# Kernel optimization log

Measured on AMD Instinct MI355X. Metric: run time of the kernel, lower is better.

## Reference

```python
import jax, jax.numpy as jnp
import numpy as np

D, K, STRIDE, PADDING = 5, 3, 1, 2
B, CIN, COUT, H, W = 32, 128, 256, 56, 56


def _conv(x, w, stride, padding):
    return jax.lax.conv_general_dilated(
        x, w, window_strides=(stride, stride),
        padding=[(padding, padding), (padding, padding)],
        dimension_numbers=("NCHW", "OIHW", "NCHW"))


def setup_inputs() -> dict:
    key = jax.random.key(0)
    k1, k2, k3 = jax.random.split(key, 3)
    x = jax.random.normal(k1, (B, CIN, H, W), dtype=jnp.float32)
    # kaiming-uniform-ish core init
    fan_in = CIN * K * K
    bound = float(np.sqrt(6.0 / fan_in))
    core = jax.random.uniform(k2, (COUT, CIN, K, K), dtype=jnp.float32,
                              minval=-bound, maxval=bound)
    periphery = jax.random.uniform(k3, (D * D - K * K,), dtype=jnp.float32,
                                   minval=-0.1, maxval=0.1)
    thresh = jnp.ones((COUT,), jnp.float32) * 0.1
    scale = jnp.array([10.0], jnp.float32)
    return {"x": x, "core": core, "periphery": periphery,
            "thresh": thresh, "scale": scale}


def reference(x, core, periphery, thresh, scale):
    pad = (D - K) // 2  # offset of the KxK core inside the DxD window
    # Dense core conv: embed KxK core at the center of a DxD kernel so core
    # and periphery share the same output grid (padding=PADDING for DxD).
    core_full = jnp.pad(core, ((0, 0), (0, 0), (pad, pad), (pad, pad)))
    core_out = _conv(x, core_full, STRIDE, PADDING)  # [B, COUT, Ho, Wo]

    # Periphery: one shared scalar per off-core offset, shared across all
    # in/out channels -> sum input over channels, conv with a 1x1-channel
    # DxD stencil whose core region is zero.
    periph_mask = np.ones((D, D), dtype=bool)
    periph_mask[pad:pad + K, pad:pad + K] = False
    periph_idx = np.flatnonzero(periph_mask)  # row-major off-core offsets
    pk = jnp.zeros((D * D,), x.dtype).at[periph_idx].set(periphery)
    pk = pk.reshape(1, 1, D, D)
    xs = jnp.sum(x, axis=1, keepdims=True)  # [B,1,H,W]
    periph_out = _conv(xs, pk, STRIDE, PADDING)  # [B,1,Ho,Wo]

    # Per-out-channel threshold/scale gating: periphery term is switched on
    # where the core response exceeds the channel threshold (soft gate).
    gate = jax.nn.sigmoid(scale[0] * (core_out - thresh[None, :, None, None]))
    return core_out + gate * periph_out
```

## Files before the change

kernel.cpp:

```cpp
#include <hip/hip_runtime.h>

typedef __attribute__((__ext_vector_type__(8))) _Float16 f16x8;
typedef __attribute__((__ext_vector_type__(4))) float f32x4;
typedef __attribute__((__ext_vector_type__(4))) int i32x4;

#define HW 56
#define HW2 3136
#define CIN 128
#define COUT 256
#define NB 32
#define NPIX 100352
#define PH 58

static __device__ __forceinline__ unsigned short f2h(float f) {
  _Float16 h = (_Float16)f;
  return __builtin_bit_cast(unsigned short, h);
}

#define GLD_LDS16(g, l)                                          \
  __builtin_amdgcn_global_load_lds(                              \
      (const __attribute__((address_space(1))) void*)(g),        \
      (__attribute__((address_space(3))) void*)(l), 16, 0, 0)

__global__ __launch_bounds__(256) void zero_halo(unsigned short* __restrict__ xp) {
  int t = blockIdx.x * 256 + threadIdx.x;
  int ck = t & 15;
  int pi = t >> 4;
  int b = pi / 228, r = pi - b * 228;
  int h, w;
  if (r < 58) { h = 0; w = r; }
  else if (r < 116) { h = 57; w = r - 58; }
  else { int q = r - 116; h = 1 + (q >> 1); w = (q & 1) * 57; }
  size_t off = (((size_t)(b * PH + h) * PH + w) << 8) + (ck << 4);
  *reinterpret_cast<i32x4*>((char*)xp + off) = (i32x4){0, 0, 0, 0};
}

__global__ __launch_bounds__(256) void prep_x(const float* __restrict__ x,
                                              unsigned short* __restrict__ xp,
                                              float* __restrict__ xs) {
  __shared__ float tile[CIN * 57];
  const int bh = blockIdx.x;
  const float* src = x + (size_t)(bh / HW) * CIN * HW2 + (size_t)(bh % HW) * HW;
  for (int idx = threadIdx.x; idx < CIN * HW; idx += 256) {
    int c = idx / HW, w = idx - c * HW;
    tile[c * 57 + w] = src[(size_t)c * HW2 + w];
  }
  __syncthreads();
  unsigned short* dst =
      xp + (((size_t)(bh / HW) * PH + (bh % HW) + 1) * PH + 1) * CIN;
  for (int idx = threadIdx.x; idx < HW * (CIN / 2); idx += 256) {
    int w = idx >> 6;
    int c = (idx & 63) << 1;
    unsigned lo = f2h(tile[c * 57 + w]);
    unsigned hi = f2h(tile[(c + 1) * 57 + w]);
    *reinterpret_cast<unsigned*>(&dst[w * CIN + c]) = lo | (hi << 16);
  }
  if (threadIdx.x < HW) {
    float s = 0.f;
    for (int c = 0; c < CIN; ++c) s += tile[c * 57 + threadIdx.x];
    xs[(size_t)bh * HW + threadIdx.x] = s;
  }
}

__global__ __launch_bounds__(256) void prep_w(const float* __restrict__ core,
                                              unsigned short* __restrict__ w_t) {
  int i = blockIdx.x * 256 + threadIdx.x;
  int c = i & 127;
  int p = (i >> 7) % 9;
  int m = i / (9 * 128);
  w_t[i] = f2h(core[(size_t)(m * CIN + c) * 9 + p]);
}

__global__ __launch_bounds__(256) void periph_k(const float* __restrict__ xs,
                                                const float* __restrict__ per,
                                                float* __restrict__ po) {
  int n = blockIdx.x * 256 + threadIdx.x;
  int b = n / HW2, r = n - b * HW2;
  int ho = r / HW, wo = r - ho * HW;
  const float* xb = xs + (size_t)b * HW2;
  const int pdy[16] = {0,0,0,0,0,1,1,2,2,3,3,4,4,4,4,4};
  const int pdx[16] = {0,1,2,3,4,0,4,0,4,0,4,0,1,2,3,4};
  float acc = 0.f;
#pragma unroll
  for (int t = 0; t < 16; ++t) {
    int h = ho + pdy[t] - 2, w = wo + pdx[t] - 2;
    if ((unsigned)h < HW && (unsigned)w < HW) acc += per[t] * xb[h * HW + w];
  }
  po[n] = acc;
}

__global__ __launch_bounds__(512, 2) void gemm_k(const unsigned short* __restrict__ xp,
                                                 const unsigned short* __restrict__ w_t,
                                                 const float* __restrict__ po,
                                                 const float* __restrict__ thresh,
                                                 const float* __restrict__ scale,
                                                 float* __restrict__ out) {
  __shared__ __align__(16) char sMem[2 * 65536 + 1024];

  const int tid = threadIdx.x;
  const int lane = tid & 63;
  const int wid = tid >> 6;
  const int wm = wid >> 2;
  const int wn = wid & 3;

  const int bid = blockIdx.x;
  const int n0 = ((bid & 7) * 49 + (bid >> 3)) << 8;

  float* sTh = (float*)(sMem + 131072);
  if (tid < 256) sTh[tid] = thresh[tid];

  const int slot = tid & 7;
  const int trow = tid >> 3;
  const int sw = (slot ^ (trow & 7)) << 4;
  const char* xpc = (const char*)xp;
  const char* wtc = (const char*)w_t;
  int aOff[4], bOff[4];
#pragma unroll
  for (int q = 0; q < 4; ++q) {
    int row = q * 64 + trow;
    aOff[q] = row * (9 * 256) + sw;
    int n = n0 + row;
    int b = n / HW2, rr = n - b * HW2;
    int h = rr / HW, w = rr - h * HW;
    bOff[q] = ((b * PH + h + 1) * PH + (w + 1)) * 256 + sw;
  }
  const int ldsw = wid * 1024;

  int aro[8][2], bro[4][2];
#pragma unroll
  for (int i = 0; i < 8; ++i)
#pragma unroll
    for (int ko = 0; ko < 2; ++ko) {
      int rowA = wm * 128 + i * 16 + (lane & 15);
      int boc = ko * 64 + ((lane >> 4) << 4);
      aro[i][ko] = rowA * 128 + (boc ^ ((rowA & 7) << 4));
    }
#pragma unroll
  for (int j = 0; j < 4; ++j)
#pragma unroll
    for (int ko = 0; ko < 2; ++ko) {
      int rowB = wn * 64 + j * 16 + (lane & 15);
      int boc = ko * 64 + ((lane >> 4) << 4);
      bro[j][ko] = 32768 + rowB * 128 + (boc ^ ((rowB & 7) << 4));
    }

  auto STAGE = [&](int buf, int step) {
    const int p = step >> 1;
    const int c0b = (step & 1) << 7;
    const int dy = p / 3 - 1, dx = p - (p / 3) * 3 - 1;
    const int offA = (p << 8) + c0b;
    const int offB = ((dy * PH + dx) << 8) + c0b;
    char* base = sMem + buf * 65536;
#pragma unroll
    for (int q = 0; q < 4; ++q)
      GLD_LDS16(wtc + aOff[q] + offA, base + ldsw + q * 8192);
#pragma unroll
    for (int q = 0; q < 4; ++q)
      GLD_LDS16(xpc + bOff[q] + offB, base + 32768 + ldsw + q * 8192);
  };

  f32x4 acc[8][4] = {};

  STAGE(0, 0);
  __syncthreads();

#pragma unroll
  for (int s = 0; s < 18; ++s) {
    const char* base = sMem + (s & 1) * 65536;
    __builtin_amdgcn_s_barrier();
    if (s < 17) {
      STAGE((s + 1) & 1, s + 1);
      asm volatile("s_waitcnt vmcnt(8)" ::: "memory");
    } else {
      asm volatile("s_waitcnt vmcnt(0)" ::: "memory");
    }
    __builtin_amdgcn_s_barrier();
    f16x8 bfr[4][2];
#pragma unroll
    for (int j = 0; j < 4; ++j)
#pragma unroll
      for (int ko = 0; ko < 2; ++ko)
        bfr[j][ko] = *reinterpret_cast<const f16x8*>(base + bro[j][ko]);
#pragma unroll
    for (int i = 0; i < 8; ++i) {
      f16x8 a0 = *reinterpret_cast<const f16x8*>(base + aro[i][0]);
      f16x8 a1 = *reinterpret_cast<const f16x8*>(base + aro[i][1]);
      __builtin_amdgcn_s_setprio(1);
#pragma unroll
      for (int j = 0; j < 4; ++j) {
        acc[i][j] = __builtin_amdgcn_mfma_f32_16x16x32_f16(a0, bfr[j][0], acc[i][j], 0, 0, 0);
        acc[i][j] = __builtin_amdgcn_mfma_f32_16x16x32_f16(a1, bfr[j][1], acc[i][j], 0, 0, 0);
      }
      __builtin_amdgcn_s_setprio(0);
    }
  }

  const float sc = scale[0];
#pragma unroll
  for (int j = 0; j < 4; ++j) {
    int n = n0 + wn * 64 + j * 16 + (lane & 15);
    int b = n / HW2;
    int r = n - b * HW2;
    float pv = po[n];
    float* op = out + (size_t)b * (COUT * HW2) + r;
#pragma unroll
    for (int i = 0; i < 8; ++i) {
      int cl = wm * 128 + i * 16 + ((lane >> 4) << 2);
#pragma unroll
      for (int q = 0; q < 4; ++q) {
        float cv = acc[i][j][q];
        float g = 1.f / (1.f + __expf(-sc * (cv - sTh[cl + q])));
        op[(size_t)(cl + q) * HW2] = cv + g * pv;
      }
    }
  }
}

extern "C" void kernel_launch(void* const* d_in, const int* in_sizes, int n_in,
                              void* d_out, int out_size, void* d_ws, size_t ws_size,
                              hipStream_t stream) {
  (void)in_sizes; (void)n_in; (void)out_size; (void)ws_size;
  const float* x      = (const float*)d_in[0];
  const float* core   = (const float*)d_in[1];
  const float* per    = (const float*)d_in[2];
  const float* thresh = (const float*)d_in[3];
  const float* scale  = (const float*)d_in[4];
  float* out = (float*)d_out;

  char* ws = (char*)d_ws;
  unsigned short* xp  = (unsigned short*)ws;
  unsigned short* w_t = (unsigned short*)(ws + 27557888);
  float* xs           = (float*)(ws + 28147712);
  float* po           = (float*)(ws + 28549120);

  zero_halo<<<(NB * 228 * 16) / 256, 256, 0, stream>>>(xp);
  prep_x<<<NB * HW, 256, 0, stream>>>(x, xp, xs);
  prep_w<<<(COUT * 9 * CIN) / 256, 256, 0, stream>>>(core, w_t);
  periph_k<<<NPIX / 256, 256, 0, stream>>>(xs, per, po);
  gemm_k<<<NPIX / 256, 512, 0, stream>>>(xp, w_t, po, thresh, scale, out);
}
```

Measured before the change: 120.5 us.

## Interleave next-tile global-to-LDS loads with MFMA sub-phases in a two-ahead prefetch

Restructures the GEMM main loop so that loads for tile t+2 are issued in pieces during the four MFMA sub-phases of tile t, into the same buffer being consumed. B halves go out after their LDS reads and A goes out after a barrier and an lgkmcnt wait. The intent is to spread memory issue across compute and keep two tiles in flight instead of one. In exchange it adds many more barriers per tile and relies on fragile vmcnt accounting and buffer-reuse ordering.

```diff
diff --git a/kernel.cpp b/kernel.cpp
--- a/kernel.cpp
+++ b/kernel.cpp
@@ -126,6 +126,25 @@
   }
   const int ldsw = wid * 1024;
 
+  auto stageA4 = [&](char* base, int offA) {
+#pragma unroll
+    for (int q = 0; q < 4; ++q)
+      GLD_LDS16(wtc + aOff[q] + offA, base + q * 8192 + ldsw);
+  };
+  auto stageB2 = [&](char* base, int offB, int half) {
+#pragma unroll
+    for (int q = 0; q < 2; ++q) {
+      int qq = half * 2 + q;
+      GLD_LDS16(xpc + bOff[qq] + offB, base + 32768 + qq * 8192 + ldsw);
+    }
+  };
+  auto tileOffA = [](int t) { return ((t >> 1) << 8) + ((t & 1) << 7); };
+  auto tileOffB = [](int t) {
+    int p = t >> 1;
+    int dy = p / 3 - 1, dx = p - (p / 3) * 3 - 1;
+    return ((dy * PH + dx) << 8) + ((t & 1) << 7);
+  };
+
   int aro[8][2], bro[4][2];
 #pragma unroll
   for (int i = 0; i < 8; ++i)
@@ -144,54 +163,69 @@
       bro[j][ko] = 32768 + rowB * 128 + (boc ^ ((rowB & 7) << 4));
     }
 
-  auto STAGE = [&](int buf, int step) {
-    const int p = step >> 1;
-    const int c0b = (step & 1) << 7;
-    const int dy = p / 3 - 1, dx = p - (p / 3) * 3 - 1;
-    const int offA = (p << 8) + c0b;
-    const int offB = ((dy * PH + dx) << 8) + c0b;
-    char* base = sMem + buf * 65536;
-#pragma unroll
-    for (int q = 0; q < 4; ++q)
-      GLD_LDS16(wtc + aOff[q] + offA, base + ldsw + q * 8192);
-#pragma unroll
-    for (int q = 0; q < 4; ++q)
-      GLD_LDS16(xpc + bOff[q] + offB, base + 32768 + ldsw + q * 8192);
-  };
-
   f32x4 acc[8][4] = {};
 
-  STAGE(0, 0);
-  __syncthreads();
-
-#pragma unroll
-  for (int s = 0; s < 18; ++s) {
-    const char* base = sMem + (s & 1) * 65536;
-    __builtin_amdgcn_s_barrier();
-    if (s < 17) {
-      STAGE((s + 1) & 1, s + 1);
-      asm volatile("s_waitcnt vmcnt(8)" ::: "memory");
-    } else {
-      asm volatile("s_waitcnt vmcnt(0)" ::: "memory");
-    }
-    __builtin_amdgcn_s_barrier();
+  stageB2(sMem, tileOffB(0), 0);
+  stageB2(sMem, tileOffB(0), 1);
+  stageA4(sMem, tileOffA(0));
+  stageB2(sMem + 65536, tileOffB(1), 0);
+  stageB2(sMem + 65536, tileOffB(1), 1);
+  stageA4(sMem + 65536, tileOffA(1));
+  asm volatile("s_waitcnt vmcnt(8)" ::: "memory");
+  __builtin_amdgcn_s_barrier();
+
+  for (int t = 0; t < 18; ++t) {
+    char* base = sMem + (t & 1) * 65536;
+    const int tn = t + 2;
+    const bool st = tn < 18;
+    const int offAN = st ? tileOffA(tn) : 0;
+    const int offBN = st ? tileOffB(tn) : 0;
+
     f16x8 bfr[4][2];
 #pragma unroll
-    for (int j = 0; j < 4; ++j)
-#pragma unroll
-      for (int ko = 0; ko < 2; ++ko)
-        bfr[j][ko] = *reinterpret_cast<const f16x8*>(base + bro[j][ko]);
-#pragma unroll
-    for (int i = 0; i < 8; ++i) {
-      f16x8 a0 = *reinterpret_cast<const f16x8*>(base + aro[i][0]);
-      f16x8 a1 = *reinterpret_cast<const f16x8*>(base + aro[i][1]);
+    for (int q = 0; q < 4; ++q) {
+      if (q == 0) {
+#pragma unroll
+        for (int j = 0; j < 4; ++j)
+#pragma unroll
+          for (int ko = 0; ko < 2; ++ko)
+            bfr[j][ko] = *reinterpret_cast<const f16x8*>(base + bro[j][ko]);
+      }
+      f16x8 aA[2][2];
+#pragma unroll
+      for (int di = 0; di < 2; ++di)
+#pragma unroll
+        for (int ko = 0; ko < 2; ++ko)
+          aA[di][ko] = *reinterpret_cast<const f16x8*>(base + aro[2 * q + di][ko]);
+
+      if (st && q == 1) stageB2(base, offBN, 0);
+      if (st && q == 2) stageB2(base, offBN, 1);
+      if (q == 3) asm volatile("s_waitcnt lgkmcnt(0)" ::: "memory");
+
+      __builtin_amdgcn_s_barrier();
+
+      if (st && q == 3) stageA4(base, offAN);
+
       __builtin_amdgcn_s_setprio(1);
 #pragma unroll
-      for (int j = 0; j < 4; ++j) {
-        acc[i][j] = __builtin_amdgcn_mfma_f32_16x16x32_f16(a0, bfr[j][0], acc[i][j], 0, 0, 0);
-        acc[i][j] = __builtin_amdgcn_mfma_f32_16x16x32_f16(a1, bfr[j][1], acc[i][j], 0, 0, 0);
+      for (int di = 0; di < 2; ++di)
+#pragma unroll
+        for (int j = 0; j < 4; ++j) {
+          acc[2 * q + di][j] =
+              __builtin_amdgcn_mfma_f32_16x16x32_f16(aA[di][0], bfr[j][0], acc[2 * q + di][j], 0, 0, 0);
+          acc[2 * q + di][j] =
+              __builtin_amdgcn_mfma_f32_16x16x32_f16(aA[di][1], bfr[j][1], acc[2 * q + di][j], 0, 0, 0);
+        }
+      __builtin_amdgcn_s_setprio(0);
+
+      if (q == 3) {
+        if (t <= 15) {
+          asm volatile("s_waitcnt vmcnt(8)" ::: "memory");
+        } else if (t == 16) {
+          asm volatile("s_waitcnt vmcnt(0)" ::: "memory");
+        }
       }
-      __builtin_amdgcn_s_setprio(0);
+      __builtin_amdgcn_s_barrier();
     }
   }
 
```

After: 122.1 us. Within noise of the previous version (+1.4%).
